# Kernel tuning notes

Measured on AMD Instinct MI355X. Metric: run time of the kernel, lower is better.

Reference implementation:

```python
import jax, jax.numpy as jnp
import numpy as np

N_HEADS = 8
HEAD_DIM = 64  # dim // n_heads = 512 // 8


def setup_inputs() -> dict:
    key = jax.random.key(0)
    ks = jax.random.split(key, 7)
    B, S, D = 2, 4096, 512
    scale = 1.0 / np.sqrt(D)
    return {
        "q": jax.random.normal(ks[0], (B, S, D), jnp.float32),
        "k": jax.random.normal(ks[1], (B, S, D), jnp.float32),
        "v": jax.random.normal(ks[2], (B, S, D), jnp.float32),
        "wq": jax.random.normal(ks[3], (D, D), jnp.float32) * scale,
        "wk": jax.random.normal(ks[4], (D, D), jnp.float32) * scale,
        "wv": jax.random.normal(ks[5], (D, D), jnp.float32) * scale,
        "wo": jax.random.normal(ks[6], (D, D), jnp.float32) * scale,
    }


def reference(q, k, v, wq, wk, wv, wo):
    B, S, _ = q.shape
    # projections (nn.Linear: x @ W^T), reshape to [B, H, S, Dh]
    def proj(x, w):
        return (x @ w.T).reshape(B, S, N_HEADS, HEAD_DIM).transpose(0, 2, 1, 3)
    xq, xk, xv = proj(q, wq), proj(k, wk), proj(v, wv)
    scores = jnp.einsum("bhqd,bhkd->bhqk", xq, xk) / jnp.sqrt(
        jnp.asarray(HEAD_DIM, xq.dtype))
    # causal mask: -inf above the diagonal
    causal = jnp.tril(jnp.ones((S, S), bool))
    scores = jnp.where(causal[None, None], scores, -jnp.inf)
    attn = jax.nn.softmax(scores.astype(jnp.float32), axis=-1).astype(xq.dtype)
    # dropout layers are identity in eval mode
    out = jnp.einsum("bhqk,bhkd->bhqd", attn, xv)
    out = out.transpose(0, 2, 1, 3).reshape(B, S, N_HEADS * HEAD_DIM)
    return out @ wo.T
```

## Files before the change

### kernel.cpp

```cpp
#include <hip/hip_runtime.h>

using f32x4 = __attribute__((ext_vector_type(4))) float;
using s16x8 = __attribute__((ext_vector_type(8))) short;
using u16   = unsigned short;
using u32   = unsigned int;
using u16x4 = __attribute__((ext_vector_type(4))) unsigned short;

#define S_LEN 4096
#define NH 8
#define DM 512
#define MROWS 8192

#define SWZ(r) ((((r) & 7)) ^ ((((r) >> 2) & 2)))

static __device__ __forceinline__ u16 f2bf(float f) {
  u32 x = __builtin_bit_cast(u32, f);
  return (u16)((x + 0x7FFFu + ((x >> 16) & 1u)) >> 16);
}

static __device__ __forceinline__ float fexp2(float x) {
#if __has_builtin(__builtin_amdgcn_exp2f)
  return __builtin_amdgcn_exp2f(x);
#else
  return exp2f(x);
#endif
}

static __device__ __forceinline__ float frcp(float x) {
#if __has_builtin(__builtin_amdgcn_rcpf)
  return __builtin_amdgcn_rcpf(x);
#else
  return 1.0f / x;
#endif
}

static __device__ __forceinline__ float dppmax16(float x) {
  int v;
  v = __builtin_amdgcn_update_dpp(0, __builtin_bit_cast(int, x), 0xB1, 0xF, 0xF, true);
  x = fmaxf(x, __builtin_bit_cast(float, v));
  v = __builtin_amdgcn_update_dpp(0, __builtin_bit_cast(int, x), 0x4E, 0xF, 0xF, true);
  x = fmaxf(x, __builtin_bit_cast(float, v));
  v = __builtin_amdgcn_update_dpp(0, __builtin_bit_cast(int, x), 0x141, 0xF, 0xF, true);
  x = fmaxf(x, __builtin_bit_cast(float, v));
  v = __builtin_amdgcn_update_dpp(0, __builtin_bit_cast(int, x), 0x140, 0xF, 0xF, true);
  x = fmaxf(x, __builtin_bit_cast(float, v));
  return x;
}

typedef __attribute__((address_space(3))) void lds_void_t;
typedef const __attribute__((address_space(1))) void gbl_void_t;

static __device__ __forceinline__ void gload16(const void* g, void* l) {
  __builtin_amdgcn_global_load_lds((gbl_void_t*)g, (lds_void_t*)l, 16, 0, 0);
}

static __device__ __forceinline__ s16x8 lds_frag(const u16* base, int row, int c) {
  return *(const s16x8*)(base + row * 64 + ((c ^ SWZ(row)) << 3));
}

__global__ void cvt_qkv(const float* __restrict__ q, const float* __restrict__ k,
                        const float* __restrict__ v, u16* __restrict__ oq,
                        u16* __restrict__ ok, u16* __restrict__ ov) {
  const int z = blockIdx.y;
  const float* in = (z == 0) ? q : (z == 1) ? k : v;
  u16* out = (z == 0) ? oq : (z == 1) ? ok : ov;
  const int i = blockIdx.x * 256 + threadIdx.x;
  float4 t = ((const float4*)in)[i];
  u16x4 o;
  o.x = f2bf(t.x); o.y = f2bf(t.y); o.z = f2bf(t.z); o.w = f2bf(t.w);
  ((u16x4*)out)[i] = o;
}

__global__ void cvt_w(const float* __restrict__ wq, const float* __restrict__ wk,
                      const float* __restrict__ wv, const float* __restrict__ wo,
                      u16* __restrict__ Wq, u16* __restrict__ Wk,
                      u16* __restrict__ Wv, u16* __restrict__ Wo) {
  const int z = blockIdx.y;
  const float* in = (z == 0) ? wq : (z == 1) ? wk : (z == 2) ? wv : wo;
  u16* out = (z == 0) ? Wq : (z == 1) ? Wk : (z == 2) ? Wv : Wo;
  const float scale = (z == 0) ? 0.18033688011112042f : 1.0f;
  const int i = blockIdx.x * 256 + threadIdx.x;
  float4 t = ((const float4*)in)[i];
  u16x4 o;
  o.x = f2bf(t.x * scale); o.y = f2bf(t.y * scale);
  o.z = f2bf(t.z * scale); o.w = f2bf(t.w * scale);
  ((u16x4*)out)[i] = o;
}

static __device__ __forceinline__ void gemm_core(const u16* __restrict__ A,
                                                 const u16* __restrict__ Bw,
                                                 int m0, int n0, int tid,
                                                 f32x4 (&acc)[2][4], u16* As, u16* Bs) {
  const int l = tid & 63, w = tid >> 6;
  const int g = l >> 4, r16 = l & 15;

  auto stage = [&](int buf, int kt) {
    const int k0 = kt * 64;
#pragma unroll
    for (int s = 0; s < 4; ++s) {
      const int idx = s * 256 + tid;
      const int r = idx >> 3;
      const int c = (idx & 7) ^ SWZ(r);
      gload16(A + (size_t)(m0 + r) * DM + k0 + c * 8, As + buf * 8192 + (s * 4 + w) * 512);
    }
#pragma unroll
    for (int s = 0; s < 2; ++s) {
      const int idx = s * 256 + tid;
      const int r = idx >> 3;
      const int c = (idx & 7) ^ SWZ(r);
      gload16(Bw + (size_t)(n0 + r) * DM + k0 + c * 8, Bs + buf * 4096 + (s * 4 + w) * 512);
    }
  };

  stage(0, 0);
  __syncthreads();
  for (int kt = 0; kt < 8; ++kt) {
    const int cur = kt & 1;
    if (kt < 7) stage(cur ^ 1, kt + 1);
    const u16* Ab = As + cur * 8192 + w * 32 * 64;
    const u16* Bb = Bs + cur * 4096;
#pragma unroll
    for (int kk = 0; kk < 2; ++kk) {
      s16x8 a0 = lds_frag(Ab, r16, kk * 4 + g);
      s16x8 a1 = lds_frag(Ab, 16 + r16, kk * 4 + g);
#pragma unroll
      for (int ni = 0; ni < 4; ++ni) {
        s16x8 bf = lds_frag(Bb, ni * 16 + r16, kk * 4 + g);
        acc[0][ni] = __builtin_amdgcn_mfma_f32_16x16x32_bf16(a0, bf, acc[0][ni], 0, 0, 0);
        acc[1][ni] = __builtin_amdgcn_mfma_f32_16x16x32_bf16(a1, bf, acc[1][ni], 0, 0, 0);
      }
    }
    __syncthreads();
  }
}

__global__ __launch_bounds__(256, 3) void proj_gemm(
    const u16* __restrict__ Xq, const u16* __restrict__ Xk, const u16* __restrict__ Xv,
    const u16* __restrict__ Wqm, const u16* __restrict__ Wkm, const u16* __restrict__ Wvm,
    u16* __restrict__ Qp, u16* __restrict__ Kp, u16* __restrict__ VTp) {
  __shared__ u16 As[2][128 * 64];
  __shared__ u16 Bs[2][64 * 64];
  const int z = blockIdx.z;
  const u16* A  = (z == 0) ? Xq : (z == 1) ? Xk : Xv;
  const u16* Bw = (z == 0) ? Wqm : (z == 1) ? Wkm : Wvm;
  const int tid = threadIdx.x;
  const int m0 = blockIdx.y * 128, n0 = blockIdx.x * 64;

  f32x4 acc[2][4];
#pragma unroll
  for (int mf = 0; mf < 2; ++mf)
#pragma unroll
    for (int ni = 0; ni < 4; ++ni) acc[mf][ni] = (f32x4){0.f, 0.f, 0.f, 0.f};

  gemm_core(A, Bw, m0, n0, tid, acc, &As[0][0], &Bs[0][0]);

  const int l = tid & 63, w = tid >> 6, g = l >> 4, r16 = l & 15;
#pragma unroll
  for (int mf = 0; mf < 2; ++mf)
#pragma unroll
    for (int ni = 0; ni < 4; ++ni)
#pragma unroll
      for (int r = 0; r < 4; ++r) {
        const int m = m0 + w * 32 + mf * 16 + 4 * g + r;
        const int n = n0 + ni * 16 + r16;
        const float v = acc[mf][ni][r];
        const int b = m >> 12, s = m & 4095;
        const int h = n >> 6, d = n & 63;
        if (z < 2) {
          u16* out = z ? Kp : Qp;
          out[((size_t)(b * NH + h) * S_LEN + s) * 64 + d] = f2bf(v);
        } else {
          VTp[((size_t)(b * NH + h) * 64 + d) * S_LEN + s] = f2bf(v);
        }
      }
}

__global__ __launch_bounds__(256, 3) void out_gemm(const u16* __restrict__ A,
                                                   const u16* __restrict__ Bw,
                                                   float* __restrict__ out) {
  __shared__ u16 As[2][128 * 64];
  __shared__ u16 Bs[2][64 * 64];
  const int tid = threadIdx.x;
  const int m0 = blockIdx.y * 128, n0 = blockIdx.x * 64;

  f32x4 acc[2][4];
#pragma unroll
  for (int mf = 0; mf < 2; ++mf)
#pragma unroll
    for (int ni = 0; ni < 4; ++ni) acc[mf][ni] = (f32x4){0.f, 0.f, 0.f, 0.f};

  gemm_core(A, Bw, m0, n0, tid, acc, &As[0][0], &Bs[0][0]);

  const int l = tid & 63, w = tid >> 6, g = l >> 4, r16 = l & 15;
#pragma unroll
  for (int mf = 0; mf < 2; ++mf)
#pragma unroll
    for (int ni = 0; ni < 4; ++ni)
#pragma unroll
      for (int r = 0; r < 4; ++r) {
        const int m = m0 + w * 32 + mf * 16 + 4 * g + r;
        const int n = n0 + ni * 16 + r16;
        out[(size_t)m * DM + n] = acc[mf][ni][r];
      }
}

__global__ __launch_bounds__(256, 3) void attn128(const u16* __restrict__ Qp,
                                                  const u16* __restrict__ Kp,
                                                  const u16* __restrict__ VTp,
                                                  u16* __restrict__ Aout) {
  __shared__ u16 Kl[2][64 * 64];
  __shared__ u16 Vl[2][64 * 64];
  __shared__ u16 Pl[4][32 * 64];

  const int tid = threadIdx.x, l = tid & 63, w = tid >> 6;
  const int g = l >> 4, r16 = l & 15;

  const int lid = blockIdx.y * 32 + blockIdx.x;
  const int pos = lid & 255, half = lid >> 8;
  const int bh = (pos >> 5) + half * 8;
  const int qi = half ? (31 - (pos & 31)) : (pos & 31);
  const int q0 = qi * 128;
  const int nt = 2 * qi + 2;

  const u16* Kbase = Kp + (size_t)bh * S_LEN * 64;
  const u16* Vbase = VTp + (size_t)bh * 64 * S_LEN;

  s16x8 aq[2][2];
#pragma unroll
  for (int m = 0; m < 2; ++m)
#pragma unroll
    for (int kk = 0; kk < 2; ++kk)
      aq[m][kk] = *(const s16x8*)(Qp + ((size_t)bh * S_LEN + q0 + w * 32 + m * 16 + r16) * 64 +
                                  kk * 32 + g * 8);

  f32x4 oacc[2][4];
  f32x4 lacc[2];
  float mrow[2][4];
#pragma unroll
  for (int m = 0; m < 2; ++m) {
    lacc[m] = (f32x4){0.f, 0.f, 0.f, 0.f};
#pragma unroll
    for (int ni = 0; ni < 4; ++ni) oacc[m][ni] = (f32x4){0.f, 0.f, 0.f, 0.f};
#pragma unroll
    for (int r = 0; r < 4; ++r) mrow[m][r] = -1e30f;
  }

  s16x8 ones;
#pragma unroll
  for (int i = 0; i < 8; ++i) ones[i] = (short)0x3F80;

  auto stage = [&](int buf, int t) {
    const int kv0 = t * 64;
#pragma unroll
    for (int s = 0; s < 2; ++s) {
      const int idx = s * 256 + tid;
      const int r = idx >> 3;
      const int c = (idx & 7) ^ SWZ(r);
      gload16(Kbase + (size_t)(kv0 + r) * 64 + c * 8, &Kl[buf][(s * 4 + w) * 512]);
      gload16(Vbase + (size_t)r * S_LEN + kv0 + c * 8, &Vl[buf][(s * 4 + w) * 512]);
    }
  };

  stage(0, 0);
  __syncthreads();

  for (int t = 0; t < nt; ++t) {
    const int cur = t & 1;
    if (t + 1 < nt) stage(cur ^ 1, t + 1);

    const u16* Kb = Kl[cur];
    const u16* Vb = Vl[cur];
    u16* Pw = Pl[w];

    f32x4 sv[2][4];
#pragma unroll
    for (int ci = 0; ci < 4; ++ci) {
      s16x8 b0 = lds_frag(Kb, ci * 16 + r16, g);
      s16x8 b1 = lds_frag(Kb, ci * 16 + r16, 4 + g);
#pragma unroll
      for (int m = 0; m < 2; ++m) {
        f32x4 tacc = (f32x4){0.f, 0.f, 0.f, 0.f};
        tacc = __builtin_amdgcn_mfma_f32_16x16x32_bf16(aq[m][0], b0, tacc, 0, 0, 0);
        tacc = __builtin_amdgcn_mfma_f32_16x16x32_bf16(aq[m][1], b1, tacc, 0, 0, 0);
        sv[m][ci] = tacc;
      }
    }

    if (t >= nt - 2) {
      const int kv0 = t * 64;
#pragma unroll
      for (int m = 0; m < 2; ++m)
#pragma unroll
        for (int ci = 0; ci < 4; ++ci)
#pragma unroll
          for (int r = 0; r < 4; ++r) {
            const int row = q0 + w * 32 + m * 16 + 4 * g + r;
            const int col = kv0 + ci * 16 + r16;
            if (col > row) sv[m][ci][r] = -1e30f;
          }
    }

#pragma unroll
    for (int m = 0; m < 2; ++m) {
      float fac[4];
#pragma unroll
      for (int r = 0; r < 4; ++r) {
        float tm = fmaxf(fmaxf(sv[m][0][r], sv[m][1][r]), fmaxf(sv[m][2][r], sv[m][3][r]));
        tm = dppmax16(tm);
        const float mnew = fmaxf(mrow[m][r], tm);
        fac[r] = fexp2(mrow[m][r] - mnew);
        mrow[m][r] = mnew;
      }
#pragma unroll
      for (int ci = 0; ci < 4; ++ci)
#pragma unroll
        for (int r = 0; r < 4; ++r) {
          const float pv = fexp2(sv[m][ci][r] - mrow[m][r]);
          const int row = m * 16 + 4 * g + r;
          const int col = ci * 16 + r16;
          Pw[row * 64 + ((col >> 3) ^ SWZ(row)) * 8 + (col & 7)] = f2bf(pv);
        }
#pragma unroll
      for (int r = 0; r < 4; ++r) {
        lacc[m][r] *= fac[r];
#pragma unroll
        for (int ni = 0; ni < 4; ++ni) oacc[m][ni][r] *= fac[r];
      }
    }

#pragma unroll
    for (int kk = 0; kk < 2; ++kk) {
      s16x8 pa0 = lds_frag(Pw, r16, kk * 4 + g);
      s16x8 pa1 = lds_frag(Pw, 16 + r16, kk * 4 + g);
      lacc[0] = __builtin_amdgcn_mfma_f32_16x16x32_bf16(pa0, ones, lacc[0], 0, 0, 0);
      lacc[1] = __builtin_amdgcn_mfma_f32_16x16x32_bf16(pa1, ones, lacc[1], 0, 0, 0);
#pragma unroll
      for (int ni = 0; ni < 4; ++ni) {
        s16x8 bv = lds_frag(Vb, ni * 16 + r16, kk * 4 + g);
        oacc[0][ni] = __builtin_amdgcn_mfma_f32_16x16x32_bf16(pa0, bv, oacc[0][ni], 0, 0, 0);
        oacc[1][ni] = __builtin_amdgcn_mfma_f32_16x16x32_bf16(pa1, bv, oacc[1][ni], 0, 0, 0);
      }
    }
    __syncthreads();
  }

  const int b = bh >> 3, h = bh & 7;
#pragma unroll
  for (int m = 0; m < 2; ++m) {
    float rn[4];
#pragma unroll
    for (int r = 0; r < 4; ++r) rn[r] = frcp(lacc[m][r]);
#pragma unroll
    for (int ni = 0; ni < 4; ++ni)
#pragma unroll
      for (int r = 0; r < 4; ++r) {
        const int s = q0 + w * 32 + m * 16 + 4 * g + r;
        const int d = ni * 16 + r16;
        Aout[((size_t)b * S_LEN + s) * DM + h * 64 + d] = f2bf(oacc[m][ni][r] * rn[r]);
      }
  }
}

extern "C" void kernel_launch(void* const* d_in, const int* in_sizes, int n_in,
                              void* d_out, int out_size, void* d_ws, size_t ws_size,
                              hipStream_t stream) {
  const float* q  = (const float*)d_in[0];
  const float* k  = (const float*)d_in[1];
  const float* v  = (const float*)d_in[2];
  const float* wq = (const float*)d_in[3];
  const float* wk = (const float*)d_in[4];
  const float* wv = (const float*)d_in[5];
  const float* wo = (const float*)d_in[6];

  char* ws = (char*)d_ws;
  u16* Xq  = (u16*)(ws + 0);
  u16* Xk  = (u16*)(ws + 8388608);
  u16* Xv  = (u16*)(ws + 16777216);
  u16* Wq  = (u16*)(ws + 25165824);
  u16* Wk  = (u16*)(ws + 25690112);
  u16* Wv  = (u16*)(ws + 26214400);
  u16* Wo  = (u16*)(ws + 26738688);
  u16* Qp  = (u16*)(ws + 27262976);
  u16* Kp  = (u16*)(ws + 35651584);
  u16* VTp = (u16*)(ws + 44040192);
  u16* Att = (u16*)(ws + 52428800);

  cvt_qkv<<<dim3(4096, 3), dim3(256), 0, stream>>>(q, k, v, Xq, Xk, Xv);
  cvt_w<<<dim3(256, 4), dim3(256), 0, stream>>>(wq, wk, wv, wo, Wq, Wk, Wv, Wo);

  proj_gemm<<<dim3(8, 64, 3), dim3(256), 0, stream>>>(Xq, Xk, Xv, Wq, Wk, Wv, Qp, Kp, VTp);

  attn128<<<dim3(32, 16), dim3(256), 0, stream>>>(Qp, Kp, VTp, Att);

  out_gemm<<<dim3(8, 64), dim3(256), 0, stream>>>(Att, Wo, (float*)d_out);
}
```

Baseline: 273.3 us.

## Enlarge GEMM tiles to 128x128, transpose V through LDS, fuse conversion kernels

The projection and output GEMMs move from 128x64 to 128x128 block tiles, with each wave computing a 64x64 sub-tile (4x4 MFMA fragments). This raises MFMA work per LDS fragment load and halves the block count. Blocks are remapped with an XCD-aware interleave, and the V-transpose epilogue now goes through a swizzled LDS buffer so the transposed stores to global are coalesced 16-byte writes. The two fp32-to-bf16 conversion kernels are merged into one launch, at the cost of idle blocks in the weight slice. The trade-off is higher register use (launch bounds drop to 2) and fewer, larger blocks, which lowers occupancy.

```diff
diff --git a/kernel.cpp b/kernel.cpp
--- a/kernel.cpp
+++ b/kernel.cpp
@@ -58,41 +58,43 @@
   return *(const s16x8*)(base + row * 64 + ((c ^ SWZ(row)) << 3));
 }
 
-__global__ void cvt_qkv(const float* __restrict__ q, const float* __restrict__ k,
-                        const float* __restrict__ v, u16* __restrict__ oq,
-                        u16* __restrict__ ok, u16* __restrict__ ov) {
+__global__ void cvt_all(const float* __restrict__ q, const float* __restrict__ k,
+                        const float* __restrict__ v, const float* __restrict__ wq,
+                        const float* __restrict__ wk, const float* __restrict__ wv,
+                        const float* __restrict__ wo, u16* __restrict__ oq,
+                        u16* __restrict__ ok, u16* __restrict__ ov, u16* __restrict__ Wq,
+                        u16* __restrict__ Wk, u16* __restrict__ Wv, u16* __restrict__ Wo) {
   const int z = blockIdx.y;
-  const float* in = (z == 0) ? q : (z == 1) ? k : v;
-  u16* out = (z == 0) ? oq : (z == 1) ? ok : ov;
-  const int i = blockIdx.x * 256 + threadIdx.x;
-  float4 t = ((const float4*)in)[i];
-  u16x4 o;
-  o.x = f2bf(t.x); o.y = f2bf(t.y); o.z = f2bf(t.z); o.w = f2bf(t.w);
-  ((u16x4*)out)[i] = o;
-}
-
-__global__ void cvt_w(const float* __restrict__ wq, const float* __restrict__ wk,
-                      const float* __restrict__ wv, const float* __restrict__ wo,
-                      u16* __restrict__ Wq, u16* __restrict__ Wk,
-                      u16* __restrict__ Wv, u16* __restrict__ Wo) {
-  const int z = blockIdx.y;
-  const float* in = (z == 0) ? wq : (z == 1) ? wk : (z == 2) ? wv : wo;
-  u16* out = (z == 0) ? Wq : (z == 1) ? Wk : (z == 2) ? Wv : Wo;
-  const float scale = (z == 0) ? 0.18033688011112042f : 1.0f;
-  const int i = blockIdx.x * 256 + threadIdx.x;
-  float4 t = ((const float4*)in)[i];
-  u16x4 o;
-  o.x = f2bf(t.x * scale); o.y = f2bf(t.y * scale);
-  o.z = f2bf(t.z * scale); o.w = f2bf(t.w * scale);
-  ((u16x4*)out)[i] = o;
+  if (z < 3) {
+    const float* in = (z == 0) ? q : (z == 1) ? k : v;
+    u16* out = (z == 0) ? oq : (z == 1) ? ok : ov;
+    const int i = blockIdx.x * 256 + threadIdx.x;
+    float4 t = ((const float4*)in)[i];
+    u16x4 o;
+    o.x = f2bf(t.x); o.y = f2bf(t.y); o.z = f2bf(t.z); o.w = f2bf(t.w);
+    ((u16x4*)out)[i] = o;
+  } else {
+    if (blockIdx.x >= 1024) return;
+    const int which = blockIdx.x >> 8;
+    const float* in = (which == 0) ? wq : (which == 1) ? wk : (which == 2) ? wv : wo;
+    u16* out = (which == 0) ? Wq : (which == 1) ? Wk : (which == 2) ? Wv : Wo;
+    const float scale = (which == 0) ? 0.18033688011112042f : 1.0f;
+    const int i = (blockIdx.x & 255) * 256 + threadIdx.x;
+    float4 t = ((const float4*)in)[i];
+    u16x4 o;
+    o.x = f2bf(t.x * scale); o.y = f2bf(t.y * scale);
+    o.z = f2bf(t.z * scale); o.w = f2bf(t.w * scale);
+    ((u16x4*)out)[i] = o;
+  }
 }
 
 static __device__ __forceinline__ void gemm_core(const u16* __restrict__ A,
                                                  const u16* __restrict__ Bw,
                                                  int m0, int n0, int tid,
-                                                 f32x4 (&acc)[2][4], u16* As, u16* Bs) {
-  const int l = tid & 63, w = tid >> 6;
+                                                 f32x4 (&acc)[4][4], u16* As, u16* Bs) {
+  const int l = tid & 63;
   const int g = l >> 4, r16 = l & 15;
+  const int w = tid >> 6, wr = w >> 1, wc = w & 1;
 
   auto stage = [&](int buf, int kt) {
     const int k0 = kt * 64;
@@ -102,13 +104,7 @@
       const int r = idx >> 3;
       const int c = (idx & 7) ^ SWZ(r);
       gload16(A + (size_t)(m0 + r) * DM + k0 + c * 8, As + buf * 8192 + (s * 4 + w) * 512);
-    }
-#pragma unroll
-    for (int s = 0; s < 2; ++s) {
-      const int idx = s * 256 + tid;
-      const int r = idx >> 3;
-      const int c = (idx & 7) ^ SWZ(r);
-      gload16(Bw + (size_t)(n0 + r) * DM + k0 + c * 8, Bs + buf * 4096 + (s * 4 + w) * 512);
+      gload16(Bw + (size_t)(n0 + r) * DM + k0 + c * 8, Bs + buf * 8192 + (s * 4 + w) * 512);
     }
   };
 
@@ -117,90 +113,128 @@
   for (int kt = 0; kt < 8; ++kt) {
     const int cur = kt & 1;
     if (kt < 7) stage(cur ^ 1, kt + 1);
-    const u16* Ab = As + cur * 8192 + w * 32 * 64;
-    const u16* Bb = Bs + cur * 4096;
+    const u16* Ab = As + cur * 8192 + wr * 64 * 64;
+    const u16* Bb = Bs + cur * 8192 + wc * 64 * 64;
 #pragma unroll
     for (int kk = 0; kk < 2; ++kk) {
-      s16x8 a0 = lds_frag(Ab, r16, kk * 4 + g);
-      s16x8 a1 = lds_frag(Ab, 16 + r16, kk * 4 + g);
-#pragma unroll
-      for (int ni = 0; ni < 4; ++ni) {
-        s16x8 bf = lds_frag(Bb, ni * 16 + r16, kk * 4 + g);
-        acc[0][ni] = __builtin_amdgcn_mfma_f32_16x16x32_bf16(a0, bf, acc[0][ni], 0, 0, 0);
-        acc[1][ni] = __builtin_amdgcn_mfma_f32_16x16x32_bf16(a1, bf, acc[1][ni], 0, 0, 0);
-      }
+      s16x8 af[4], bf[4];
+#pragma unroll
+      for (int mi = 0; mi < 4; ++mi) af[mi] = lds_frag(Ab, mi * 16 + r16, kk * 4 + g);
+#pragma unroll
+      for (int ni = 0; ni < 4; ++ni) bf[ni] = lds_frag(Bb, ni * 16 + r16, kk * 4 + g);
+#pragma unroll
+      for (int mi = 0; mi < 4; ++mi)
+#pragma unroll
+        for (int ni = 0; ni < 4; ++ni)
+          acc[mi][ni] = __builtin_amdgcn_mfma_f32_16x16x32_bf16(af[mi], bf[ni], acc[mi][ni], 0, 0, 0);
     }
     __syncthreads();
   }
 }
 
-__global__ __launch_bounds__(256, 3) void proj_gemm(
+__global__ __launch_bounds__(256, 2) void proj_gemm(
     const u16* __restrict__ Xq, const u16* __restrict__ Xk, const u16* __restrict__ Xv,
     const u16* __restrict__ Wqm, const u16* __restrict__ Wkm, const u16* __restrict__ Wvm,
     u16* __restrict__ Qp, u16* __restrict__ Kp, u16* __restrict__ VTp) {
-  __shared__ u16 As[2][128 * 64];
-  __shared__ u16 Bs[2][64 * 64];
-  const int z = blockIdx.z;
+  __shared__ u16 As[2][8192];
+  __shared__ u16 Bs[2][8192];
+  const int bid = blockIdx.x;
+  const int logical = (bid & 7) * 96 + (bid >> 3);
+  const int z = logical >> 8;
+  const int rr = logical & 255;
+  const int by = rr >> 2, bx = rr & 3;
+  const int m0 = by * 128, n0 = bx * 128;
+
   const u16* A  = (z == 0) ? Xq : (z == 1) ? Xk : Xv;
   const u16* Bw = (z == 0) ? Wqm : (z == 1) ? Wkm : Wvm;
   const int tid = threadIdx.x;
-  const int m0 = blockIdx.y * 128, n0 = blockIdx.x * 64;
-
-  f32x4 acc[2][4];
-#pragma unroll
-  for (int mf = 0; mf < 2; ++mf)
-#pragma unroll
-    for (int ni = 0; ni < 4; ++ni) acc[mf][ni] = (f32x4){0.f, 0.f, 0.f, 0.f};
+
+  f32x4 acc[4][4];
+#pragma unroll
+  for (int mi = 0; mi < 4; ++mi)
+#pragma unroll
+    for (int ni = 0; ni < 4; ++ni) acc[mi][ni] = (f32x4){0.f, 0.f, 0.f, 0.f};
 
   gemm_core(A, Bw, m0, n0, tid, acc, &As[0][0], &Bs[0][0]);
 
   const int l = tid & 63, w = tid >> 6, g = l >> 4, r16 = l & 15;
-#pragma unroll
-  for (int mf = 0; mf < 2; ++mf)
-#pragma unroll
-    for (int ni = 0; ni < 4; ++ni)
-#pragma unroll
-      for (int r = 0; r < 4; ++r) {
-        const int m = m0 + w * 32 + mf * 16 + 4 * g + r;
-        const int n = n0 + ni * 16 + r16;
-        const float v = acc[mf][ni][r];
-        const int b = m >> 12, s = m & 4095;
+  const int wr = w >> 1, wc = w & 1;
+
+  if (z < 2) {
+    u16* out = z ? Kp : Qp;
+#pragma unroll
+    for (int mi = 0; mi < 4; ++mi)
+#pragma unroll
+      for (int ni = 0; ni < 4; ++ni) {
+        const int n = n0 + wc * 64 + ni * 16 + r16;
         const int h = n >> 6, d = n & 63;
-        if (z < 2) {
-          u16* out = z ? Kp : Qp;
-          out[((size_t)(b * NH + h) * S_LEN + s) * 64 + d] = f2bf(v);
-        } else {
-          VTp[((size_t)(b * NH + h) * 64 + d) * S_LEN + s] = f2bf(v);
+#pragma unroll
+        for (int r = 0; r < 4; ++r) {
+          const int m = m0 + wr * 64 + mi * 16 + 4 * g + r;
+          const int b = m >> 12, s = m & 4095;
+          out[((size_t)(b * NH + h) * S_LEN + s) * 64 + d] = f2bf(acc[mi][ni][r]);
         }
       }
-}
-
-__global__ __launch_bounds__(256, 3) void out_gemm(const u16* __restrict__ A,
+  } else {
+    u16* Tt = &As[0][0];
+#pragma unroll
+    for (int mi = 0; mi < 4; ++mi)
+#pragma unroll
+      for (int ni = 0; ni < 4; ++ni) {
+        const int n = wc * 64 + ni * 16 + r16;
+        const int mb = wr * 64 + mi * 16 + 4 * g;
+        const int ad = n * 128 + (((mb >> 3) ^ (n & 15)) << 3) + (mb & 7);
+        Tt[ad + 0] = f2bf(acc[mi][ni][0]);
+        Tt[ad + 1] = f2bf(acc[mi][ni][1]);
+        Tt[ad + 2] = f2bf(acc[mi][ni][2]);
+        Tt[ad + 3] = f2bf(acc[mi][ni][3]);
+      }
+    __syncthreads();
+    const int b0 = m0 >> 12;
+    const int srow0 = m0 & 4095;
+    const int h0 = bx * 2;
+#pragma unroll
+    for (int it = 0; it < 8; ++it) {
+      const int n = it * 16 + (tid >> 4);
+      const int mc = tid & 15;
+      s16x8 vch = *(const s16x8*)&Tt[n * 128 + ((mc ^ (n & 15)) << 3)];
+      u16* dst = VTp + ((size_t)(b0 * NH + h0 + (n >> 6)) * 64 + (n & 63)) * S_LEN +
+                 srow0 + mc * 8;
+      *(s16x8*)dst = vch;
+    }
+  }
+}
+
+__global__ __launch_bounds__(256, 2) void out_gemm(const u16* __restrict__ A,
                                                    const u16* __restrict__ Bw,
                                                    float* __restrict__ out) {
-  __shared__ u16 As[2][128 * 64];
-  __shared__ u16 Bs[2][64 * 64];
+  __shared__ u16 As[2][8192];
+  __shared__ u16 Bs[2][8192];
+  const int bid = blockIdx.x;
+  const int logical = (bid & 7) * 32 + (bid >> 3);
+  const int by = logical >> 2, bx = logical & 3;
+  const int m0 = by * 128, n0 = bx * 128;
   const int tid = threadIdx.x;
-  const int m0 = blockIdx.y * 128, n0 = blockIdx.x * 64;
-
-  f32x4 acc[2][4];
-#pragma unroll
-  for (int mf = 0; mf < 2; ++mf)
-#pragma unroll
-    for (int ni = 0; ni < 4; ++ni) acc[mf][ni] = (f32x4){0.f, 0.f, 0.f, 0.f};
+
+  f32x4 acc[4][4];
+#pragma unroll
+  for (int mi = 0; mi < 4; ++mi)
+#pragma unroll
+    for (int ni = 0; ni < 4; ++ni) acc[mi][ni] = (f32x4){0.f, 0.f, 0.f, 0.f};
 
   gemm_core(A, Bw, m0, n0, tid, acc, &As[0][0], &Bs[0][0]);
 
   const int l = tid & 63, w = tid >> 6, g = l >> 4, r16 = l & 15;
-#pragma unroll
-  for (int mf = 0; mf < 2; ++mf)
+  const int wr = w >> 1, wc = w & 1;
+#pragma unroll
+  for (int mi = 0; mi < 4; ++mi)
 #pragma unroll
     for (int ni = 0; ni < 4; ++ni)
 #pragma unroll
       for (int r = 0; r < 4; ++r) {
-        const int m = m0 + w * 32 + mf * 16 + 4 * g + r;
-        const int n = n0 + ni * 16 + r16;
-        out[(size_t)m * DM + n] = acc[mf][ni][r];
+        const int m = m0 + wr * 64 + mi * 16 + 4 * g + r;
+        const int n = n0 + wc * 64 + ni * 16 + r16;
+        out[(size_t)m * DM + n] = acc[mi][ni][r];
       }
 }
 
@@ -385,12 +419,12 @@
   u16* VTp = (u16*)(ws + 44040192);
   u16* Att = (u16*)(ws + 52428800);
 
-  cvt_qkv<<<dim3(4096, 3), dim3(256), 0, stream>>>(q, k, v, Xq, Xk, Xv);
-  cvt_w<<<dim3(256, 4), dim3(256), 0, stream>>>(wq, wk, wv, wo, Wq, Wk, Wv, Wo);
-
-  proj_gemm<<<dim3(8, 64, 3), dim3(256), 0, stream>>>(Xq, Xk, Xv, Wq, Wk, Wv, Qp, Kp, VTp);
+  cvt_all<<<dim3(4096, 4), dim3(256), 0, stream>>>(q, k, v, wq, wk, wv, wo,
+                                                   Xq, Xk, Xv, Wq, Wk, Wv, Wo);
+
+  proj_gemm<<<dim3(768), dim3(256), 0, stream>>>(Xq, Xk, Xv, Wq, Wk, Wv, Qp, Kp, VTp);
 
   attn128<<<dim3(32, 16), dim3(256), 0, stream>>>(Qp, Kp, VTp, Att);
 
-  out_gemm<<<dim3(8, 64), dim3(256), 0, stream>>>(Att, Wo, (float*)d_out);
-}
+  out_gemm<<<dim3(256), dim3(256), 0, stream>>>(Att, Wo, (float*)d_out);
+}
```

Measured after the change: 246.7 us. 1.11x faster.
